# Optimization experiments

Measured on AMD Instinct MI355X. Metric: run time of the kernel, lower is better.

The kernel has to match this reference:

```python
import jax, jax.numpy as jnp
import numpy as np

N_SRC = 16384   # src nodes in block (includes dst nodes first, per DGL convention)
N_DST = 8192    # dst nodes
K = 32          # fixed in-degree per dst node -> dense mailbox [N_DST, K]
E = N_DST * K   # 262144 edges; edge i has dst node i // K
T = 16          # padded edge-sequence length
NODE_IN = 64
H = 64          # node_hidden_dim
E_IN = 8        # edge_in_dim
TH = 8          # time_hidden_dim
D_IN = E_IN + TH


def lstm_last(x, lengths, Wih, Whh, bih, bhh):
    """Unidirectional 1-layer LSTM; returns hidden state at step lengths-1 (pack_padded h_n).
    x: (E, T, D); lengths: (E,) in [1, T]. PyTorch gate order: i, f, g, o."""
    n, t_max, _ = x.shape
    h0 = jnp.zeros((n, H), x.dtype)

    def step(carry, xt):
        h, c, hlast, t = carry
        g = xt @ Wih.T + bih + h @ Whh.T + bhh
        i, f, gg, o = jnp.split(g, 4, axis=-1)
        c = jax.nn.sigmoid(f) * c + jax.nn.sigmoid(i) * jnp.tanh(gg)
        h = jax.nn.sigmoid(o) * jnp.tanh(c)
        hlast = jnp.where((t < lengths)[:, None], h, hlast)
        return (h, c, hlast, t + 1), None

    init = (h0, h0, h0, jnp.int32(0))
    (_, _, hlast, _), _ = jax.lax.scan(step, init, jnp.swapaxes(x, 0, 1))
    return hlast  # (E, H)


def sparsemax(z):
    """Sparsemax over last axis (Martins & Astudillo), matching the torch code."""
    z = z - jnp.max(z, axis=-1, keepdims=True)
    zs = -jnp.sort(-z, axis=-1)  # descending
    r = jnp.arange(1, z.shape[-1] + 1, dtype=z.dtype)
    bound = 1.0 + r * zs
    cs = jnp.cumsum(zs, axis=-1)
    is_gt = (bound > cs).astype(z.dtype)
    k = jnp.max(is_gt * r, axis=-1, keepdims=True)
    taus = (jnp.sum(is_gt * zs, axis=-1, keepdims=True) - 1.0) / k
    return jnp.maximum(z - taus, 0.0)


def setup_inputs():
    key = jax.random.key(0)
    ks = jax.random.split(key, 24)
    s = 0.1
    inp = {}
    inp["node_features"] = jax.random.normal(ks[0], (N_SRC, NODE_IN), jnp.float32)
    inp["edge_feats"] = jax.random.normal(ks[1], (E, T, E_IN), jnp.float32)
    inp["e_times"] = jax.random.uniform(ks[2], (E, T), jnp.float32)
    inp["e_len"] = jax.random.randint(ks[3], (E,), 1, T + 1).astype(jnp.int32)
    inp["edge_src"] = jax.random.randint(ks[4], (E,), 0, N_SRC).astype(jnp.int32)
    # Time2Vec (SineActivation) params: v = cat([sin(tau@w + b), tau@w0 + b0])
    inp["t2v_w"] = s * jax.random.normal(ks[5], (1, TH - 1), jnp.float32)
    inp["t2v_b"] = s * jax.random.normal(ks[6], (1, TH - 1), jnp.float32)
    inp["t2v_w0"] = s * jax.random.normal(ks[7], (1, 1), jnp.float32)
    inp["t2v_b0"] = s * jax.random.normal(ks[8], (1, 1), jnp.float32)
    # edge_layer LSTM
    inp["lstm_e_Wih"] = s * jax.random.normal(ks[9], (4 * H, D_IN), jnp.float32)
    inp["lstm_e_Whh"] = s * jax.random.normal(ks[10], (4 * H, H), jnp.float32)
    inp["lstm_e_bih"] = s * jax.random.normal(ks[11], (4 * H,), jnp.float32)
    inp["lstm_e_bhh"] = s * jax.random.normal(ks[12], (4 * H,), jnp.float32)
    # edge_attn_layer LSTM
    inp["lstm_a_Wih"] = s * jax.random.normal(ks[13], (4 * H, D_IN), jnp.float32)
    inp["lstm_a_Whh"] = s * jax.random.normal(ks[14], (4 * H, H), jnp.float32)
    inp["lstm_a_bih"] = s * jax.random.normal(ks[15], (4 * H,), jnp.float32)
    inp["lstm_a_bhh"] = s * jax.random.normal(ks[16], (4 * H,), jnp.float32)
    # attention scorer (no bias), edge_out and node linears
    inp["attn_w"] = s * jax.random.normal(ks[17], (H, 1), jnp.float32)
    inp["edge_out_W"] = s * jax.random.normal(ks[18], (H, NODE_IN + H), jnp.float32)
    inp["edge_out_b"] = s * jax.random.normal(ks[19], (H,), jnp.float32)
    inp["node_W"] = s * jax.random.normal(ks[20], (H, NODE_IN + H), jnp.float32)
    inp["node_b"] = s * jax.random.normal(ks[21], (H,), jnp.float32)
    return inp


def reference(node_features, edge_feats, e_times, t2v_w, t2v_b, t2v_w0, t2v_b0,
              lstm_e_Wih, lstm_e_Whh, lstm_e_bih, lstm_e_bhh,
              lstm_a_Wih, lstm_a_Whh, lstm_a_bih, lstm_a_bhh,
              attn_w, edge_out_W, edge_out_b, node_W, node_b,
              e_len, edge_src):
    h_src = node_features                 # dropout is identity in eval
    h_dst = node_features[:N_DST]
    # Time2Vec: tau (E, T, 1) -> (E, T, TH)
    tau = e_times[..., None]
    tenc = jnp.concatenate([jnp.sin(tau * t2v_w[0] + t2v_b[0]),
                            tau * t2v_w0[0] + t2v_b0[0]], axis=-1)
    e = jnp.concatenate([edge_feats, tenc], axis=-1)  # (E, T, D_IN)
    # per-edge LSTM encodings (last valid step)
    e_out = lstm_last(e, e_len, lstm_e_Wih, lstm_e_Whh, lstm_e_bih, lstm_e_bhh)  # (E, H)
    a_out = lstm_last(e, e_len, lstm_a_Wih, lstm_a_Whh, lstm_a_bih, lstm_a_bhh)  # (E, H)
    a = jax.nn.leaky_relu(a_out @ attn_w, 0.01)  # (E, 1)
    # per-edge message
    m = jax.nn.relu(jnp.concatenate([h_src[edge_src], e_out], axis=-1) @ edge_out_W.T + edge_out_b)  # (E, H)
    # reduce over ragged mailbox (regular degree K -> dense [N_DST, K, H])
    mb = m.reshape(N_DST, K, H)
    alpha = sparsemax(a.reshape(N_DST, K))[..., None]  # (N_DST, K, 1)
    h_neigh = jnp.sum(alpha * mb, axis=1)              # (N_DST, H)
    h = jax.nn.relu(jnp.concatenate([h_dst, h_neigh], axis=-1) @ node_W.T + node_b)
    return h  # (N_DST, H)
```

## Files before the change

### kernel.cpp

```cpp
#include <hip/hip_runtime.h>

typedef __bf16 bf16;
typedef __bf16 bf16x8 __attribute__((ext_vector_type(8)));
typedef float f32x4 __attribute__((ext_vector_type(4)));

#define N_DSTN 8192
#define TT 16
#define HROW 72
#define HBUF (32 * HROW)

__device__ __forceinline__ f32x4 MFMA(bf16x8 a, bf16x8 b, f32x4 c) {
    return __builtin_amdgcn_mfma_f32_16x16x32_bf16(a, b, c, 0, 0, 0);
}
__device__ __forceinline__ float ldf(const void* p, long i, bool isb) {
    return isb ? (float)((const bf16*)p)[i] : ((const float*)p)[i];
}
__device__ __forceinline__ bf16x8 zero8() {
    bf16x8 z;
    #pragma unroll
    for (int i = 0; i < 8; i++) z[i] = (bf16)0.0f;
    return z;
}
__device__ __forceinline__ bf16x8 ld8v(const void* p, long i, bool isb) {
    if (isb) {
        return *reinterpret_cast<const bf16x8*>((const bf16*)p + i);
    } else {
        const float* f = (const float*)p + i;
        float4 u = *reinterpret_cast<const float4*>(f);
        float4 v = *reinterpret_cast<const float4*>(f + 4);
        bf16x8 r;
        r[0] = (bf16)u.x; r[1] = (bf16)u.y; r[2] = (bf16)u.z; r[3] = (bf16)u.w;
        r[4] = (bf16)v.x; r[5] = (bf16)v.y; r[6] = (bf16)v.z; r[7] = (bf16)v.w;
        return r;
    }
}
__device__ __forceinline__ bf16x8 ld8vs(const void* p, long i, bool isb, float s) {
    bf16x8 r;
    if (isb) {
        bf16x8 v = *reinterpret_cast<const bf16x8*>((const bf16*)p + i);
        #pragma unroll
        for (int j = 0; j < 8; j++) r[j] = (bf16)((float)v[j] * s);
    } else {
        const float* f = (const float*)p + i;
        float4 u = *reinterpret_cast<const float4*>(f);
        float4 v = *reinterpret_cast<const float4*>(f + 4);
        r[0] = (bf16)(u.x * s); r[1] = (bf16)(u.y * s); r[2] = (bf16)(u.z * s); r[3] = (bf16)(u.w * s);
        r[4] = (bf16)(v.x * s); r[5] = (bf16)(v.y * s); r[6] = (bf16)(v.z * s); r[7] = (bf16)(v.w * s);
    }
    return r;
}

extern "C" __global__ void __launch_bounds__(512, 4)
gtea_fused(const void* __restrict__ node_features,
           const void* __restrict__ edge_feats,
           const void* __restrict__ e_times,
           const int*  __restrict__ e_len,
           const int*  __restrict__ edge_src,
           const void* __restrict__ t2v_w,
           const void* __restrict__ t2v_b,
           const void* __restrict__ t2v_w0,
           const void* __restrict__ t2v_b0,
           const void* __restrict__ Wih_e,
           const void* __restrict__ Whh_e,
           const void* __restrict__ bih_e,
           const void* __restrict__ bhh_e,
           const void* __restrict__ Wih_a,
           const void* __restrict__ Whh_a,
           const void* __restrict__ bih_a,
           const void* __restrict__ bhh_a,
           const void* __restrict__ attn_w,
           const void* __restrict__ edge_out_W,
           const void* __restrict__ edge_out_b,
           const void* __restrict__ node_W,
           const void* __restrict__ node_b,
           void* __restrict__ outp)
{
    __shared__ __align__(16) bf16 habuf[2][2][HBUF];
    __shared__ __align__(16) bf16 hsrc[32 * HROW];
    __shared__ __align__(16) bf16 featb[TT * 32 * 8];
    __shared__ __align__(16) bf16 tb[TT * 32 * 8];
    __shared__ float t2w[8], t2b[8];
    __shared__ float attn_f[64];
    __shared__ float vbuf[128];
    __shared__ float scores_sh[32], alpha_sh[32];
    __shared__ int   lens_sh[32], idx_sh[32];
    __shared__ int   isb_sh;

    const int tid = threadIdx.x;
    const int w   = tid >> 6;
    const int l   = tid & 63;
    const int l15 = l & 15;
    const int q   = l >> 4;
    const int L   = w >> 2;
    const int w4  = w & 3;
    const int u16 = w4 * 16 + l15;

    const int d  = blockIdx.x;
    const int e0 = d * 32;

    if (tid < 64) {
        const unsigned short* u = (const unsigned short*)e_times;
        unsigned short a = u[tid * 2], b = u[tid * 2 + 1];
        bool ok = (a <= 0x3F80u) && (b <= 0x3F80u);
        unsigned long long m = __ballot(ok);
        if (tid == 0) isb_sh = (m == ~0ULL) ? 1 : 0;
    }
    if (tid < 32) {
        int lj = e_len[e0 + tid];
        int rank = 0;
        for (int i = 0; i < 32; i++) {
            int li = __shfl(lj, i);
            rank += (li > lj) || (li == lj && i < tid);
        }
        int mt = rank >> 4, kp = rank & 15;
        int slot = mt * 16 + (kp & 3) * 4 + (kp >> 2);
        idx_sh[slot]  = tid;
        lens_sh[slot] = lj;
    }
    __syncthreads();
    const bool isb = (isb_sh != 0);

    if (tid < 7)  { t2w[tid] = ldf(t2v_w, tid, isb); t2b[tid] = ldf(t2v_b, tid, isb); }
    if (tid == 7) { t2w[7] = ldf(t2v_w0, 0, isb); t2b[7] = ldf(t2v_b0, 0, isb); }
    if (tid < 64) attn_f[tid] = ldf(attn_w, tid, isb);
    if (tid < 64) vbuf[tid] = ldf(node_features, (long)d * 64 + tid, isb);
    {
        unsigned int* hz = reinterpret_cast<unsigned int*>(&habuf[0][0][0]);
        for (int i = tid; i < 2 * 2 * HBUF / 2; i += 512) hz[i] = 0u;
    }
    __syncthreads();

    int gm0[4], gm1[4];
    #pragma unroll
    for (int r = 0; r < 4; r++) {
        gm0[r] = __builtin_amdgcn_readfirstlane(lens_sh[r]);
        gm1[r] = __builtin_amdgcn_readfirstlane(lens_sh[16 + r]);
    }
    const int tmax = gm0[0], mtmax1 = gm1[0];

    unsigned lp = 0;
    #pragma unroll
    for (int mt = 0; mt < 2; mt++)
        #pragma unroll
        for (int r = 0; r < 4; r++)
            lp |= (unsigned)(lens_sh[mt * 16 + q * 4 + r] - 1) << ((mt * 4 + r) * 4);

    if (tid < 256) {
        int s = tid >> 3, c8 = tid & 7;
        int src = edge_src[e0 + idx_sh[s]];
        *reinterpret_cast<bf16x8*>(&hsrc[s * HROW + c8 * 8]) =
            ld8v(node_features, (long)src * 64 + c8 * 8, isb);
    }
    {
        int s = tid >> 4, t = tid & 15;
        int j = idx_sh[s];
        long base = ((long)(e0 + j) * TT + t) * 8;
        *reinterpret_cast<bf16x8*>(&featb[(t * 32 + s) * 8]) = ld8v(edge_feats, base, isb);
        float tau = ldf(e_times, (long)(e0 + j) * TT + t, isb);
        bf16x8 te;
        #pragma unroll
        for (int i = 0; i < 7; i++) te[i] = (bf16)__sinf(tau * t2w[i] + t2b[i]);
        te[7] = (bf16)(tau * t2w[7] + t2b[7]);
        *reinterpret_cast<bf16x8*>(&tb[(t * 32 + s) * 8]) = te;
    }

    const void* Whh = L ? Whh_a : Whh_e;
    const void* Wih = L ? Wih_a : Wih_e;
    const void* bih = L ? bih_a : bih_e;
    const void* bhh = L ? bhh_a : bhh_e;
    bf16x8 Bh[4][2], Bx[4];
    float  bias[4];
    #pragma unroll
    for (int j = 0; j < 4; j++) {
        const float gs = (j == 2) ? 2.88539008f : -1.44269504f;
        int n = 64 * j + u16;
        Bh[j][0] = ld8vs(Whh, (long)n * 64 + q * 8, isb, gs);
        Bh[j][1] = ld8vs(Whh, (long)n * 64 + 32 + q * 8, isb, gs);
        Bx[j] = (q < 2) ? ld8vs(Wih, (long)n * 16 + q * 8, isb, gs) : zero8();
        bias[j] = (ldf(bih, n, isb) + ldf(bhh, n, isb)) * gs;
    }

    float c[2][4];
    #pragma unroll
    for (int mt = 0; mt < 2; mt++)
        #pragma unroll
        for (int r = 0; r < 4; r++) c[mt][r] = 0.0f;

    __syncthreads();

    bf16* hb_base = &habuf[L][0][0];
    const int rd_off = l15 * HROW + q * 8;
    const int wr_off = (q * 4) * HROW + u16;

    for (int t = 0; t < tmax; t++) {
        const bf16* hbR = hb_base + (t & 1) * HBUF;
        bf16*       hbW = hb_base + ((t + 1) & 1) * HBUF;

        auto do_mt = [&](int mt) {
            const bf16* hr = hbR + mt * (16 * HROW) + rd_off;
            bf16x8 ah0 = *reinterpret_cast<const bf16x8*>(hr);
            bf16x8 ah1 = *reinterpret_cast<const bf16x8*>(hr + 32);
            bf16x8 xa;
            if (q < 2) {
                const bf16* xp = (q == 0 ? featb : tb) + (t * 32 + mt * 16 + l15) * 8;
                xa = *reinterpret_cast<const bf16x8*>(xp);
            } else {
                xa = zero8();
            }
            f32x4 D[4];
            #pragma unroll
            for (int j = 0; j < 4; j++) {
                f32x4 acc = {bias[j], bias[j], bias[j], bias[j]};
                acc = MFMA(ah0, Bh[j][0], acc);
                acc = MFMA(ah1, Bh[j][1], acc);
                acc = MFMA(xa,  Bx[j],    acc);
                D[j] = acc;
            }
            bf16* hw = hbW + mt * (16 * HROW) + wr_off;
            #pragma unroll
            for (int r = 0; r < 4; r++) {
                int gmax = mt ? gm1[r] : gm0[r];
                if (t < gmax) {
                    int lm1 = (int)((lp >> ((mt * 4 + r) * 4)) & 15u);
                    if (t <= lm1) {
                        float gi = D[0][r], gf = D[1][r];
                        float gg = D[2][r], go = D[3][r];
                        float ei = __builtin_amdgcn_exp2f(gi);
                        float ef = __builtin_amdgcn_exp2f(gf);
                        float eg = __builtin_amdgcn_exp2f(gg);
                        float di = 1.0f + ei, dfv = 1.0f + ef, dg = 1.0f + eg;
                        float m1 = di * dg;
                        float R1 = __builtin_amdgcn_rcpf(m1 * dfv);
                        float cn = (m1 * R1) * c[mt][r] + (eg - 1.0f) * (dfv * R1);
                        c[mt][r] = cn;
                        float eo = __builtin_amdgcn_exp2f(go);
                        float ec = __builtin_amdgcn_exp2f(2.88539008f * cn);
                        float R2 = __builtin_amdgcn_rcpf((1.0f + eo) * (1.0f + ec));
                        float hn = (ec - 1.0f) * R2;
                        hw[r * HROW] = (bf16)hn;
                    }
                }
            }
        };
        do_mt(0);
        if (t < mtmax1) do_mt(1);
        __syncthreads();
    }

    if (tid < 256) {
        int s = tid >> 3, c8 = tid & 7;
        const bf16* ha = &habuf[1][lens_sh[s] & 1][s * HROW];
        float p = 0.0f;
        #pragma unroll
        for (int i = 0; i < 8; i++)
            p += (float)ha[c8 * 8 + i] * attn_f[c8 * 8 + i];
        p += __shfl_xor(p, 1);
        p += __shfl_xor(p, 2);
        p += __shfl_xor(p, 4);
        if (c8 == 0) scores_sh[s] = (p > 0.0f) ? p : 0.01f * p;
    }
    float mval[2][4];
    if (tid < 256) {
        bf16x8 Bw[4];
        #pragma unroll
        for (int ks = 0; ks < 4; ks++)
            Bw[ks] = ld8v(edge_out_W, (long)u16 * 128 + ks * 32 + q * 8, isb);
        float mb = ldf(edge_out_b, u16, isb);
        #pragma unroll
        for (int mt = 0; mt < 2; mt++) {
            int s = mt * 16 + l15;
            const bf16* hs = &hsrc[s * HROW];
            const bf16* he = &habuf[0][lens_sh[s] & 1][s * HROW];
            bf16x8 a0 = *reinterpret_cast<const bf16x8*>(hs + q * 8);
            bf16x8 a1 = *reinterpret_cast<const bf16x8*>(hs + 32 + q * 8);
            bf16x8 a2 = *reinterpret_cast<const bf16x8*>(he + q * 8);
            bf16x8 a3 = *reinterpret_cast<const bf16x8*>(he + 32 + q * 8);
            f32x4 acc = {mb, mb, mb, mb};
            acc = MFMA(a0, Bw[0], acc);
            acc = MFMA(a1, Bw[1], acc);
            acc = MFMA(a2, Bw[2], acc);
            acc = MFMA(a3, Bw[3], acc);
            #pragma unroll
            for (int r = 0; r < 4; r++) mval[mt][r] = fmaxf(acc[r], 0.0f);
        }
    }
    __syncthreads();

    if (tid < 64) {
        float z = (tid < 32) ? scores_sh[tid] : -3.0e38f;
        float zm = z;
        #pragma unroll
        for (int m = 32; m >= 1; m >>= 1) zm = fmaxf(zm, __shfl_xor(zm, m));
        z -= zm;
        int cnt = 0; float sb = 0.0f;
        for (int i = 0; i < 32; i++) {
            float zi = __shfl(z, i);
            bool before = (zi > z) || (zi == z && i < tid);
            if (before) { cnt++; sb += zi; }
        }
        float r = (float)(cnt + 1);
        float S = sb + z;
        bool isgt = (tid < 32) && (1.0f + r * z > S);
        float kf  = isgt ? r : 0.0f;
        float sgt = isgt ? z : 0.0f;
        #pragma unroll
        for (int m = 32; m >= 1; m >>= 1) kf = fmaxf(kf, __shfl_xor(kf, m));
        #pragma unroll
        for (int m = 32; m >= 1; m >>= 1) sgt += __shfl_xor(sgt, m);
        float tau = (sgt - 1.0f) / fmaxf(kf, 1.0f);
        if (tid < 32) alpha_sh[tid] = fmaxf(z - tau, 0.0f);
    }
    __syncthreads();

    if (tid < 256) {
        float hn = 0.0f;
        #pragma unroll
        for (int mt = 0; mt < 2; mt++)
            #pragma unroll
            for (int r = 0; r < 4; r++)
                hn += alpha_sh[mt * 16 + q * 4 + r] * mval[mt][r];
        hn += __shfl_xor(hn, 16);
        hn += __shfl_xor(hn, 32);
        if (q == 0) vbuf[64 + u16] = hn;
    }
    __syncthreads();

    if (tid < 256) {
        int u = tid >> 2, kq = tid & 3;
        bf16x8 wv0 = ld8v(node_W, (long)u * 128 + kq * 32, isb);
        bf16x8 wv1 = ld8v(node_W, (long)u * 128 + kq * 32 + 8, isb);
        bf16x8 wv2 = ld8v(node_W, (long)u * 128 + kq * 32 + 16, isb);
        bf16x8 wv3 = ld8v(node_W, (long)u * 128 + kq * 32 + 24, isb);
        float acc = 0.0f;
        #pragma unroll
        for (int i = 0; i < 8; i++) {
            acc += (float)wv0[i] * vbuf[kq * 32 + i];
            acc += (float)wv1[i] * vbuf[kq * 32 + 8 + i];
            acc += (float)wv2[i] * vbuf[kq * 32 + 16 + i];
            acc += (float)wv3[i] * vbuf[kq * 32 + 24 + i];
        }
        acc += __shfl_xor(acc, 1);
        acc += __shfl_xor(acc, 2);
        if (kq == 0) {
            float s = acc + ldf(node_b, u, isb);
            float v = fmaxf(s, 0.0f);
            long o = (long)d * 64 + u;
            if (isb) ((bf16*)outp)[o] = (bf16)v;
            else     ((float*)outp)[o] = v;
        }
    }
}

extern "C" void kernel_launch(void* const* d_in, const int* in_sizes, int n_in,
                              void* d_out, int out_size, void* d_ws, size_t ws_size,
                              hipStream_t stream) {
    gtea_fused<<<N_DSTN, 512, 0, stream>>>(
        d_in[0], d_in[1], d_in[2],
        (const int*)d_in[3], (const int*)d_in[4],
        d_in[5], d_in[6], d_in[7], d_in[8],
        d_in[9], d_in[10], d_in[11], d_in[12],
        d_in[13], d_in[14], d_in[15], d_in[16],
        d_in[17], d_in[18], d_in[19],
        d_in[20], d_in[21],
        d_out);
}
```

Before: 761.2 us.

## Pre-convert weights to bf16 in a prep kernel and drop hsrc shared buffer

Adds a small prep kernel that converts and pre-scales all LSTM, edge and node weights, biases and Time2Vec parameters into a bf16/f32 workspace once per call. The main fused kernel then loads these directly instead of converting and scaling per block. It also removes the hsrc shared-memory staging, loading source-node features straight from global memory in the message MFMA, and zeroes only the habuf regions that need it. This cuts per-block conversion work and LDS use, possibly raising occupancy, at the cost of an extra launch and uncoalesced gathers in the message stage.

```diff
diff --git a/kernel.cpp b/kernel.cpp
--- a/kernel.cpp
+++ b/kernel.cpp
@@ -8,6 +8,17 @@
 #define TT 16
 #define HROW 72
 #define HBUF (32 * HROW)
+
+#define WS_WHH  0
+#define WS_WIH  65536
+#define WS_BIAS 81920
+#define WS_EW   83968
+#define WS_NW   100352
+#define WS_EB   116736
+#define WS_NB   116992
+#define WS_ATTN 117248
+#define WS_T2W  117504
+#define WS_T2B  117536
 
 __device__ __forceinline__ f32x4 MFMA(bf16x8 a, bf16x8 b, f32x4 c) {
     return __builtin_amdgcn_mfma_f32_16x16x32_bf16(a, b, c, 0, 0, 0);
@@ -34,20 +45,78 @@
         return r;
     }
 }
-__device__ __forceinline__ bf16x8 ld8vs(const void* p, long i, bool isb, float s) {
-    bf16x8 r;
-    if (isb) {
-        bf16x8 v = *reinterpret_cast<const bf16x8*>((const bf16*)p + i);
-        #pragma unroll
-        for (int j = 0; j < 8; j++) r[j] = (bf16)((float)v[j] * s);
-    } else {
-        const float* f = (const float*)p + i;
-        float4 u = *reinterpret_cast<const float4*>(f);
-        float4 v = *reinterpret_cast<const float4*>(f + 4);
-        r[0] = (bf16)(u.x * s); r[1] = (bf16)(u.y * s); r[2] = (bf16)(u.z * s); r[3] = (bf16)(u.w * s);
-        r[4] = (bf16)(v.x * s); r[5] = (bf16)(v.y * s); r[6] = (bf16)(v.z * s); r[7] = (bf16)(v.w * s);
-    }
-    return r;
+
+extern "C" __global__ void gtea_prep(const void* __restrict__ e_times,
+                                     const void* __restrict__ t2v_w,
+                                     const void* __restrict__ t2v_b,
+                                     const void* __restrict__ t2v_w0,
+                                     const void* __restrict__ t2v_b0,
+                                     const void* __restrict__ Wih_e,
+                                     const void* __restrict__ Whh_e,
+                                     const void* __restrict__ bih_e,
+                                     const void* __restrict__ bhh_e,
+                                     const void* __restrict__ Wih_a,
+                                     const void* __restrict__ Whh_a,
+                                     const void* __restrict__ bih_a,
+                                     const void* __restrict__ bhh_a,
+                                     const void* __restrict__ attn_w,
+                                     const void* __restrict__ edge_out_W,
+                                     const void* __restrict__ edge_out_b,
+                                     const void* __restrict__ node_W,
+                                     const void* __restrict__ node_b,
+                                     void* __restrict__ ws)
+{
+    __shared__ int isb_s;
+    const int tid = threadIdx.x;
+    if (tid < 64) {
+        const unsigned short* u = (const unsigned short*)e_times;
+        unsigned short a = u[tid * 2], b = u[tid * 2 + 1];
+        bool ok = (a <= 0x3F80u) && (b <= 0x3F80u);
+        unsigned long long m = __ballot(ok);
+        if (tid == 0) isb_s = (m == ~0ULL) ? 1 : 0;
+    }
+    __syncthreads();
+    const bool isb = (isb_s != 0);
+    char* wsb = (char*)ws;
+    const int gstep = blockDim.x * gridDim.x;
+    const int g0 = blockIdx.x * blockDim.x + tid;
+
+    for (int i = g0; i < 2 * 256 * 64; i += gstep) {
+        int Lw = i >> 14, rem = i & 16383, n = rem >> 6;
+        const void* W = Lw ? Whh_a : Whh_e;
+        float gs = ((n >> 6) == 2) ? 2.88539008f : -1.44269504f;
+        ((bf16*)(wsb + WS_WHH))[i] = (bf16)(ldf(W, rem, isb) * gs);
+    }
+    for (int i = g0; i < 2 * 256 * 16; i += gstep) {
+        int Lw = i >> 12, rem = i & 4095, n = rem >> 4;
+        const void* W = Lw ? Wih_a : Wih_e;
+        float gs = ((n >> 6) == 2) ? 2.88539008f : -1.44269504f;
+        ((bf16*)(wsb + WS_WIH))[i] = (bf16)(ldf(W, rem, isb) * gs);
+    }
+    for (int i = g0; i < 2 * 256; i += gstep) {
+        int Lw = i >> 8, n = i & 255;
+        const void* bi = Lw ? bih_a : bih_e;
+        const void* bh = Lw ? bhh_a : bhh_e;
+        float gs = ((n >> 6) == 2) ? 2.88539008f : -1.44269504f;
+        ((float*)(wsb + WS_BIAS))[i] = (ldf(bi, n, isb) + ldf(bh, n, isb)) * gs;
+    }
+    for (int i = g0; i < 64 * 128; i += gstep) {
+        ((bf16*)(wsb + WS_EW))[i] = (bf16)ldf(edge_out_W, i, isb);
+        ((bf16*)(wsb + WS_NW))[i] = (bf16)ldf(node_W, i, isb);
+    }
+    for (int i = g0; i < 64; i += gstep) {
+        ((float*)(wsb + WS_EB))[i]   = ldf(edge_out_b, i, isb);
+        ((float*)(wsb + WS_NB))[i]   = ldf(node_b, i, isb);
+        ((float*)(wsb + WS_ATTN))[i] = ldf(attn_w, i, isb);
+    }
+    if (g0 < 7) {
+        ((float*)(wsb + WS_T2W))[g0] = ldf(t2v_w, g0, isb);
+        ((float*)(wsb + WS_T2B))[g0] = ldf(t2v_b, g0, isb);
+    }
+    if (g0 == 7) {
+        ((float*)(wsb + WS_T2W))[7] = ldf(t2v_w0, 0, isb);
+        ((float*)(wsb + WS_T2B))[7] = ldf(t2v_b0, 0, isb);
+    }
 }
 
 extern "C" __global__ void __launch_bounds__(512, 4)
@@ -56,27 +125,10 @@
            const void* __restrict__ e_times,
            const int*  __restrict__ e_len,
            const int*  __restrict__ edge_src,
-           const void* __restrict__ t2v_w,
-           const void* __restrict__ t2v_b,
-           const void* __restrict__ t2v_w0,
-           const void* __restrict__ t2v_b0,
-           const void* __restrict__ Wih_e,
-           const void* __restrict__ Whh_e,
-           const void* __restrict__ bih_e,
-           const void* __restrict__ bhh_e,
-           const void* __restrict__ Wih_a,
-           const void* __restrict__ Whh_a,
-           const void* __restrict__ bih_a,
-           const void* __restrict__ bhh_a,
-           const void* __restrict__ attn_w,
-           const void* __restrict__ edge_out_W,
-           const void* __restrict__ edge_out_b,
-           const void* __restrict__ node_W,
-           const void* __restrict__ node_b,
+           const void* __restrict__ ws,
            void* __restrict__ outp)
 {
     __shared__ __align__(16) bf16 habuf[2][2][HBUF];
-    __shared__ __align__(16) bf16 hsrc[32 * HROW];
     __shared__ __align__(16) bf16 featb[TT * 32 * 8];
     __shared__ __align__(16) bf16 tb[TT * 32 * 8];
     __shared__ float t2w[8], t2b[8];
@@ -97,6 +149,7 @@
 
     const int d  = blockIdx.x;
     const int e0 = d * 32;
+    const char* wsb = (const char*)ws;
 
     if (tid < 64) {
         const unsigned short* u = (const unsigned short*)e_times;
@@ -120,13 +173,13 @@
     __syncthreads();
     const bool isb = (isb_sh != 0);
 
-    if (tid < 7)  { t2w[tid] = ldf(t2v_w, tid, isb); t2b[tid] = ldf(t2v_b, tid, isb); }
-    if (tid == 7) { t2w[7] = ldf(t2v_w0, 0, isb); t2b[7] = ldf(t2v_b0, 0, isb); }
-    if (tid < 64) attn_f[tid] = ldf(attn_w, tid, isb);
+    if (tid < 8)  { t2w[tid] = ((const float*)(wsb + WS_T2W))[tid];
+                    t2b[tid] = ((const float*)(wsb + WS_T2B))[tid]; }
+    if (tid < 64) attn_f[tid] = ((const float*)(wsb + WS_ATTN))[tid];
     if (tid < 64) vbuf[tid] = ldf(node_features, (long)d * 64 + tid, isb);
     {
         unsigned int* hz = reinterpret_cast<unsigned int*>(&habuf[0][0][0]);
-        for (int i = tid; i < 2 * 2 * HBUF / 2; i += 512) hz[i] = 0u;
+        for (int i = tid; i < HBUF / 2; i += 512) { hz[i] = 0u; hz[i + HBUF] = 0u; }
     }
     __syncthreads();
 
@@ -145,12 +198,6 @@
         for (int r = 0; r < 4; r++)
             lp |= (unsigned)(lens_sh[mt * 16 + q * 4 + r] - 1) << ((mt * 4 + r) * 4);
 
-    if (tid < 256) {
-        int s = tid >> 3, c8 = tid & 7;
-        int src = edge_src[e0 + idx_sh[s]];
-        *reinterpret_cast<bf16x8*>(&hsrc[s * HROW + c8 * 8]) =
-            ld8v(node_features, (long)src * 64 + c8 * 8, isb);
-    }
     {
         int s = tid >> 4, t = tid & 15;
         int j = idx_sh[s];
@@ -164,20 +211,18 @@
         *reinterpret_cast<bf16x8*>(&tb[(t * 32 + s) * 8]) = te;
     }
 
-    const void* Whh = L ? Whh_a : Whh_e;
-    const void* Wih = L ? Wih_a : Wih_e;
-    const void* bih = L ? bih_a : bih_e;
-    const void* bhh = L ? bhh_a : bhh_e;
+    const bf16*  wWhh  = (const bf16*)(wsb + WS_WHH) + (long)L * 256 * 64;
+    const bf16*  wWih  = (const bf16*)(wsb + WS_WIH) + (long)L * 256 * 16;
+    const float* wBias = (const float*)(wsb + WS_BIAS) + L * 256;
     bf16x8 Bh[4][2], Bx[4];
     float  bias[4];
     #pragma unroll
     for (int j = 0; j < 4; j++) {
-        const float gs = (j == 2) ? 2.88539008f : -1.44269504f;
         int n = 64 * j + u16;
-        Bh[j][0] = ld8vs(Whh, (long)n * 64 + q * 8, isb, gs);
-        Bh[j][1] = ld8vs(Whh, (long)n * 64 + 32 + q * 8, isb, gs);
-        Bx[j] = (q < 2) ? ld8vs(Wih, (long)n * 16 + q * 8, isb, gs) : zero8();
-        bias[j] = (ldf(bih, n, isb) + ldf(bhh, n, isb)) * gs;
+        Bh[j][0] = *reinterpret_cast<const bf16x8*>(wWhh + (long)n * 64 + q * 8);
+        Bh[j][1] = *reinterpret_cast<const bf16x8*>(wWhh + (long)n * 64 + 32 + q * 8);
+        Bx[j] = (q < 2) ? *reinterpret_cast<const bf16x8*>(wWih + (long)n * 16 + q * 8) : zero8();
+        bias[j] = wBias[n];
     }
 
     float c[2][4];
@@ -261,18 +306,19 @@
     }
     float mval[2][4];
     if (tid < 256) {
+        const bf16* wEW = (const bf16*)(wsb + WS_EW);
         bf16x8 Bw[4];
         #pragma unroll
         for (int ks = 0; ks < 4; ks++)
-            Bw[ks] = ld8v(edge_out_W, (long)u16 * 128 + ks * 32 + q * 8, isb);
-        float mb = ldf(edge_out_b, u16, isb);
+            Bw[ks] = *reinterpret_cast<const bf16x8*>(wEW + (long)u16 * 128 + ks * 32 + q * 8);
+        float mb = ((const float*)(wsb + WS_EB))[u16];
         #pragma unroll
         for (int mt = 0; mt < 2; mt++) {
             int s = mt * 16 + l15;
-            const bf16* hs = &hsrc[s * HROW];
+            int src = edge_src[e0 + idx_sh[s]];
+            bf16x8 a0 = ld8v(node_features, (long)src * 64 + q * 8, isb);
+            bf16x8 a1 = ld8v(node_features, (long)src * 64 + 32 + q * 8, isb);
             const bf16* he = &habuf[0][lens_sh[s] & 1][s * HROW];
-            bf16x8 a0 = *reinterpret_cast<const bf16x8*>(hs + q * 8);
-            bf16x8 a1 = *reinterpret_cast<const bf16x8*>(hs + 32 + q * 8);
             bf16x8 a2 = *reinterpret_cast<const bf16x8*>(he + q * 8);
             bf16x8 a3 = *reinterpret_cast<const bf16x8*>(he + 32 + q * 8);
             f32x4 acc = {mb, mb, mb, mb};
@@ -327,10 +373,11 @@
 
     if (tid < 256) {
         int u = tid >> 2, kq = tid & 3;
-        bf16x8 wv0 = ld8v(node_W, (long)u * 128 + kq * 32, isb);
-        bf16x8 wv1 = ld8v(node_W, (long)u * 128 + kq * 32 + 8, isb);
-        bf16x8 wv2 = ld8v(node_W, (long)u * 128 + kq * 32 + 16, isb);
-        bf16x8 wv3 = ld8v(node_W, (long)u * 128 + kq * 32 + 24, isb);
+        const bf16* wNW = (const bf16*)(wsb + WS_NW);
+        bf16x8 wv0 = *reinterpret_cast<const bf16x8*>(wNW + (long)u * 128 + kq * 32);
+        bf16x8 wv1 = *reinterpret_cast<const bf16x8*>(wNW + (long)u * 128 + kq * 32 + 8);
+        bf16x8 wv2 = *reinterpret_cast<const bf16x8*>(wNW + (long)u * 128 + kq * 32 + 16);
+        bf16x8 wv3 = *reinterpret_cast<const bf16x8*>(wNW + (long)u * 128 + kq * 32 + 24);
         float acc = 0.0f;
         #pragma unroll
         for (int i = 0; i < 8; i++) {
@@ -342,7 +389,7 @@
         acc += __shfl_xor(acc, 1);
         acc += __shfl_xor(acc, 2);
         if (kq == 0) {
-            float s = acc + ldf(node_b, u, isb);
+            float s = acc + ((const float*)(wsb + WS_NB))[u];
             float v = fmaxf(s, 0.0f);
             long o = (long)d * 64 + u;
             if (isb) ((bf16*)outp)[o] = (bf16)v;
@@ -354,13 +401,16 @@
 extern "C" void kernel_launch(void* const* d_in, const int* in_sizes, int n_in,
                               void* d_out, int out_size, void* d_ws, size_t ws_size,
                               hipStream_t stream) {
-    gtea_fused<<<N_DSTN, 512, 0, stream>>>(
-        d_in[0], d_in[1], d_in[2],
-        (const int*)d_in[3], (const int*)d_in[4],
+    gtea_prep<<<32, 256, 0, stream>>>(
+        d_in[2],
         d_in[5], d_in[6], d_in[7], d_in[8],
         d_in[9], d_in[10], d_in[11], d_in[12],
         d_in[13], d_in[14], d_in[15], d_in[16],
         d_in[17], d_in[18], d_in[19],
         d_in[20], d_in[21],
-        d_out);
-}
+        d_ws);
+    gtea_fused<<<N_DSTN, 512, 0, stream>>>(
+        d_in[0], d_in[1], d_in[2],
+        (const int*)d_in[3], (const int*)d_in[4],
+        d_ws, d_out);
+}
```

New measurement: 714.5 us. -6.1%, faster.
